# Kernel optimization log

Measured on AMD Instinct MI355X. Metric: run time of the kernel, lower is better.

## Reference

```python
import jax, jax.numpy as jnp
import numpy as np

B, H, S, D = 4, 16, 2048, 64
SCALE = D ** -0.5

def setup_inputs() -> dict:
    key = jax.random.key(0)
    kq, kk, kv = jax.random.split(key, 3)
    q = jax.random.normal(kq, (B, H, S, D), dtype=jnp.float32)
    k = jax.random.normal(kk, (B, H, S, D), dtype=jnp.float32)
    v = jax.random.normal(kv, (B, H, S, D), dtype=jnp.float32)
    return {"q": q, "k": k, "v": v}

def reference(q, k, v):
    # scores: [B, H, S, S]
    scores = jnp.einsum('bhqd,bhkd->bhqk', q, k) * SCALE
    attn = jax.nn.softmax(scores, axis=-1)
    # dropout is identity in eval mode (reference baseline)
    out = jnp.einsum('bhqk,bhkd->bhqd', attn, v)
    return out
```

## Files before the change

### kernel.cpp

```cpp
#include <hip/hip_runtime.h>
#include <hip/hip_bf16.h>


constexpr int Bb = 4, Hh = 16, Ss = 2048, Dd = 64;
constexpr float SCALE_LOG2E = 0.125f * 1.4426950408889634f;
constexpr int KVB = 64;
constexpr int NT = Ss / KVB;

typedef __bf16 bf16x8 __attribute__((ext_vector_type(8)));
typedef float  f32x4  __attribute__((ext_vector_type(4)));
typedef float  f32x16 __attribute__((ext_vector_type(16)));
typedef unsigned int u32x4 __attribute__((ext_vector_type(4)));

__device__ __forceinline__ unsigned cvtpk(float lo, float hi) {
  unsigned r;
  asm("v_cvt_pk_bf16_f32 %0, %1, %2" : "=v"(r) : "v"(lo), "v"(hi));
  return r;
}
__device__ __forceinline__ void permswap(unsigned &a, unsigned &b) {
  asm("v_permlane32_swap_b32 %0, %1" : "+v"(a), "+v"(b));
}

__global__ __launch_bounds__(512, 4)
void sdpa_fwd(const float* __restrict__ Qg, const float* __restrict__ Kg,
              const float* __restrict__ Vg, float* __restrict__ Og) {
  __shared__ __align__(16) char smem[33792];

  const int tid = threadIdx.x;
  const int wave = tid >> 6, lane = tid & 63;
  const int lq = lane & 31, hi = lane >> 5;
  const int swz = (lq & 7) << 4;

  const int bh = blockIdx.x * 8 + (blockIdx.y >> 3);
  const int qt = blockIdx.y & 7;
  const size_t base = (size_t)bh * (Ss * Dd);
  const int qw = qt * 256 + wave * 32;

  const float* Qp = Qg + base;
  const float* Kp = Kg + base;
  const float* Vp = Vg + base;

  const bool isK = (wave < 4);
  const int st  = tid & 255;
  const int skv = st >> 2, s4 = st & 3;
  const int r2  = st >> 3, s8 = st & 7;

  int roff[4];
#pragma unroll
  for (int ds = 0; ds < 4; ++ds) roff[ds] = (32 * ds + 16 * hi) ^ swz;

  bf16x8 qf[4];
  {
    const float* qp = Qp + (size_t)(qw + lq) * Dd;
#pragma unroll
    for (int ds = 0; ds < 4; ++ds) {
      f32x4 x0 = *(const f32x4*)(qp + 16 * ds + 8 * hi);
      f32x4 x1 = *(const f32x4*)(qp + 16 * ds + 8 * hi + 4);
#pragma unroll
      for (int j = 0; j < 4; ++j) {
        qf[ds][j]     = (__bf16)(x0[j] * SCALE_LOG2E);
        qf[ds][j + 4] = (__bf16)(x1[j] * SCALE_LOG2E);
      }
    }
  }

  f32x16 o[2];
#pragma unroll
  for (int a = 0; a < 2; ++a)
#pragma unroll
    for (int i = 0; i < 16; ++i) o[a][i] = 0.f;
  float ps = 0.f;

  f32x4 stg[4];

  auto issue = [&](int t) {
    if (isK) {
      const float* kp = Kp + (size_t)(t * KVB + skv) * Dd + 16 * s4;
#pragma unroll
      for (int i = 0; i < 4; ++i) stg[i] = *(const f32x4*)(kp + 4 * i);
    } else {
      const float* vp = Vp + (size_t)(t * KVB + 2 * r2) * Dd + s8;
#pragma unroll
      for (int j = 0; j < 8; ++j) {
        stg[j >> 2][j & 3]       = vp[8 * j];
        stg[2 + (j >> 2)][j & 3] = vp[Dd + 8 * j];
      }
    }
  };
  auto stage = [&](int buf) {
    char* kb = smem + buf * 8192;
    char* vb = smem + 16384 + buf * 8192;
    if (isK) {
#pragma unroll
      for (int c = 0; c < 2; ++c) {
        bf16x8 w;
#pragma unroll
        for (int j = 0; j < 4; ++j) {
          w[j]     = (__bf16)stg[2 * c][j];
          w[j + 4] = (__bf16)stg[2 * c + 1][j];
        }
        *(bf16x8*)(kb + skv * 128 + 16 * ((2 * s4 + c) ^ (skv & 7))) = w;
      }
    } else {
#pragma unroll
      for (int j = 0; j < 8; ++j) {
        int d = s8 + 8 * j;
        *(unsigned*)(vb + d * 128 + ((4 * r2) ^ ((d & 7) << 4))) =
            cvtpk(stg[j >> 2][j & 3], stg[2 + (j >> 2)][j & 3]);
      }
    }
  };

  issue(0);
  stage(0);
  __syncthreads();

  int pb = 0;
  for (int t = 0; t < NT; ++t) {
    const bool more = (t + 1 < NT);
    if (more) issue(t + 1);

    const char* kb = smem + pb * 8192;
    const char* vb = smem + 16384 + pb * 8192;

#pragma unroll
    for (int kvb = 0; kvb < 2; ++kvb) {
      f32x16 s;
#pragma unroll
      for (int i = 0; i < 16; ++i) s[i] = 0.f;
      __builtin_amdgcn_s_setprio(1);
#pragma unroll
      for (int ds = 0; ds < 4; ++ds) {
        bf16x8 k0 = *(const bf16x8*)(kb + (32 * kvb + lq) * 128 + roff[ds]);
        s = __builtin_amdgcn_mfma_f32_32x32x16_bf16(k0, qf[ds], s, 0, 0, 0);
      }
      __builtin_amdgcn_s_setprio(0);

#pragma unroll
      for (int i = 0; i < 16; ++i) s[i] = __builtin_amdgcn_exp2f(s[i]);
      {
        float u0 = 0.f, u1 = 0.f, u2 = 0.f, u3 = 0.f;
#pragma unroll
        for (int i = 0; i < 16; i += 4) {
          u0 += s[i]; u1 += s[i + 1]; u2 += s[i + 2]; u3 += s[i + 3];
        }
        ps += (u0 + u1) + (u2 + u3);
      }
      bf16x8 pf2[2];
#pragma unroll
      for (int h = 0; h < 2; ++h) {
        const int ofs = 8 * h;
        unsigned x0 = cvtpk(s[ofs + 0], s[ofs + 1]);
        unsigned x1 = cvtpk(s[ofs + 2], s[ofs + 3]);
        unsigned y0 = cvtpk(s[ofs + 4], s[ofs + 5]);
        unsigned y1 = cvtpk(s[ofs + 6], s[ofs + 7]);
        permswap(x0, y0);
        permswap(x1, y1);
        u32x4 w; w[0] = x0; w[1] = x1; w[2] = y0; w[3] = y1;
        pf2[h] = __builtin_bit_cast(bf16x8, w);
      }

      __builtin_amdgcn_s_setprio(1);
#pragma unroll
      for (int c = 0; c < 2; ++c) {
        const int ks = 2 * kvb + c;
        bf16x8 v0 = *(const bf16x8*)(vb + lq * 128        + roff[ks]);
        bf16x8 v1 = *(const bf16x8*)(vb + (32 + lq) * 128 + roff[ks]);
        o[0] = __builtin_amdgcn_mfma_f32_32x32x16_bf16(v0, pf2[c], o[0], 0, 0, 0);
        o[1] = __builtin_amdgcn_mfma_f32_32x32x16_bf16(v1, pf2[c], o[1], 0, 0, 0);
      }
      __builtin_amdgcn_s_setprio(0);
    }

    if (more) stage(1 - pb);
    __syncthreads();
    pb ^= 1;
  }

  const float inv = 1.0f / (ps + __shfl_xor(ps, 32));
  float* ot = (float*)smem + wave * (32 * 33);
  const int q2 = lane >> 1, c2 = lane & 1;
#pragma unroll
  for (int db = 0; db < 2; ++db) {
    const f32x16& acc = o[db];
#pragma unroll
    for (int r = 0; r < 16; ++r)
      ot[lq * 33 + ((r & 3) + 8 * (r >> 2) + 4 * hi)] = acc[r] * inv;
    float* orow = Og + base + (size_t)(qw + q2) * Dd + 32 * db + 16 * c2;
#pragma unroll
    for (int j = 0; j < 4; ++j) {
      f32x4 w;
#pragma unroll
      for (int jj = 0; jj < 4; ++jj) w[jj] = ot[q2 * 33 + 16 * c2 + 4 * j + jj];
      *(f32x4*)(orow + 4 * j) = w;
    }
  }
}

extern "C" void kernel_launch(void* const* d_in, const int* in_sizes, int n_in,
                              void* d_out, int out_size, void* d_ws, size_t ws_size,
                              hipStream_t stream) {
  const float* q = (const float*)d_in[0];
  const float* k = (const float*)d_in[1];
  const float* v = (const float*)d_in[2];
  float* o = (float*)d_out;
  dim3 grid(8, 64);
  sdpa_fwd<<<grid, dim3(512), 0, stream>>>(q, k, v, o);
}
```

Before: 92.35 us.

## Halve block to four waves with each thread loading both K and V tiles

Blocks shrink from 8 waves (256 queries) to 4 waves (128 queries) and the grid doubles to 1024 blocks. Every thread now stages both a K chunk and a V chunk instead of splitting the K and V staging across wave groups. The K conversion uses packed bf16 conversion instructions. This gives more blocks for better CU balance but doubles the K/V global traffic per query, since each KV tile is now shared by fewer queries. It also raises per-thread register pressure, and the occupancy hint changes.

```diff
diff --git a/kernel.cpp b/kernel.cpp
--- a/kernel.cpp
+++ b/kernel.cpp
@@ -21,29 +21,27 @@
   asm("v_permlane32_swap_b32 %0, %1" : "+v"(a), "+v"(b));
 }
 
-__global__ __launch_bounds__(512, 4)
+__global__ __launch_bounds__(256, 3)
 void sdpa_fwd(const float* __restrict__ Qg, const float* __restrict__ Kg,
               const float* __restrict__ Vg, float* __restrict__ Og) {
-  __shared__ __align__(16) char smem[33792];
+  __shared__ __align__(16) char smem[32768];
 
   const int tid = threadIdx.x;
   const int wave = tid >> 6, lane = tid & 63;
   const int lq = lane & 31, hi = lane >> 5;
   const int swz = (lq & 7) << 4;
 
-  const int bh = blockIdx.x * 8 + (blockIdx.y >> 3);
-  const int qt = blockIdx.y & 7;
+  const int bh = blockIdx.x * 8 + (blockIdx.y >> 4);
+  const int qt = blockIdx.y & 15;
   const size_t base = (size_t)bh * (Ss * Dd);
-  const int qw = qt * 256 + wave * 32;
+  const int qw = qt * 128 + wave * 32;
 
   const float* Qp = Qg + base;
   const float* Kp = Kg + base;
   const float* Vp = Vg + base;
 
-  const bool isK = (wave < 4);
-  const int st  = tid & 255;
-  const int skv = st >> 2, s4 = st & 3;
-  const int r2  = st >> 3, s8 = st & 7;
+  const int skv = tid >> 2, s4 = tid & 3;
+  const int r2  = tid >> 3, s8 = tid & 7;
 
   int roff[4];
 #pragma unroll
@@ -71,43 +69,32 @@
     for (int i = 0; i < 16; ++i) o[a][i] = 0.f;
   float ps = 0.f;
 
-  f32x4 stg[4];
+  f32x4 kr[4]; float vA[8], vB[8];
 
   auto issue = [&](int t) {
-    if (isK) {
-      const float* kp = Kp + (size_t)(t * KVB + skv) * Dd + 16 * s4;
+    const float* kp = Kp + (size_t)(t * KVB + skv) * Dd + 16 * s4;
 #pragma unroll
-      for (int i = 0; i < 4; ++i) stg[i] = *(const f32x4*)(kp + 4 * i);
-    } else {
-      const float* vp = Vp + (size_t)(t * KVB + 2 * r2) * Dd + s8;
+    for (int i = 0; i < 4; ++i) kr[i] = *(const f32x4*)(kp + 4 * i);
+    const float* vp = Vp + (size_t)(t * KVB + 2 * r2) * Dd + s8;
 #pragma unroll
-      for (int j = 0; j < 8; ++j) {
-        stg[j >> 2][j & 3]       = vp[8 * j];
-        stg[2 + (j >> 2)][j & 3] = vp[Dd + 8 * j];
-      }
-    }
+    for (int j = 0; j < 8; ++j) { vA[j] = vp[8 * j]; vB[j] = vp[Dd + 8 * j]; }
   };
   auto stage = [&](int buf) {
     char* kb = smem + buf * 8192;
     char* vb = smem + 16384 + buf * 8192;
-    if (isK) {
 #pragma unroll
-      for (int c = 0; c < 2; ++c) {
-        bf16x8 w;
+    for (int c = 0; c < 2; ++c) {
+      u32x4 u;
+      u[0] = cvtpk(kr[2 * c][0], kr[2 * c][1]);
+      u[1] = cvtpk(kr[2 * c][2], kr[2 * c][3]);
+      u[2] = cvtpk(kr[2 * c + 1][0], kr[2 * c + 1][1]);
+      u[3] = cvtpk(kr[2 * c + 1][2], kr[2 * c + 1][3]);
+      *(u32x4*)(kb + skv * 128 + 16 * ((2 * s4 + c) ^ (skv & 7))) = u;
+    }
 #pragma unroll
-        for (int j = 0; j < 4; ++j) {
-          w[j]     = (__bf16)stg[2 * c][j];
-          w[j + 4] = (__bf16)stg[2 * c + 1][j];
-        }
-        *(bf16x8*)(kb + skv * 128 + 16 * ((2 * s4 + c) ^ (skv & 7))) = w;
-      }
-    } else {
-#pragma unroll
-      for (int j = 0; j < 8; ++j) {
-        int d = s8 + 8 * j;
-        *(unsigned*)(vb + d * 128 + ((4 * r2) ^ ((d & 7) << 4))) =
-            cvtpk(stg[j >> 2][j & 3], stg[2 + (j >> 2)][j & 3]);
-      }
+    for (int j = 0; j < 8; ++j) {
+      int d = s8 + 8 * j;
+      *(unsigned*)(vb + d * 128 + ((4 * r2) ^ ((d & 7) << 4))) = cvtpk(vA[j], vB[j]);
     }
   };
 
@@ -204,6 +191,6 @@
   const float* k = (const float*)d_in[1];
   const float* v = (const float*)d_in[2];
   float* o = (float*)d_out;
-  dim3 grid(8, 64);
-  sdpa_fwd<<<grid, dim3(512), 0, stream>>>(q, k, v, o);
+  dim3 grid(8, 128);
+  sdpa_fwd<<<grid, dim3(256), 0, stream>>>(q, k, v, o);
 }
```

Result: slower. 107.9 us (+16.8%).

## Double KV tile to 128 rows with split half-tile prefetch staging

Applied to the files above, without the earlier changes.

Raises the KV tile size from 64 to 128 rows, which halves the number of loop iterations and block-wide barriers. Each tile's global loads are split into two halves whose issue and LDS staging are interleaved between compute quarters, so prefetch latency overlaps with MFMA work without adding staging registers. The V layout in LDS moves to a 256-byte row stride, and K conversion now uses packed cvt instructions. LDS use grows to 64 KB per block, which may reduce the number of resident blocks per CU.

```diff
diff --git a/kernel.cpp b/kernel.cpp
--- a/kernel.cpp
+++ b/kernel.cpp
@@ -4,7 +4,7 @@
 
 constexpr int Bb = 4, Hh = 16, Ss = 2048, Dd = 64;
 constexpr float SCALE_LOG2E = 0.125f * 1.4426950408889634f;
-constexpr int KVB = 64;
+constexpr int KVB = 128;
 constexpr int NT = Ss / KVB;
 
 typedef __bf16 bf16x8 __attribute__((ext_vector_type(8)));
@@ -24,7 +24,7 @@
 __global__ __launch_bounds__(512, 4)
 void sdpa_fwd(const float* __restrict__ Qg, const float* __restrict__ Kg,
               const float* __restrict__ Vg, float* __restrict__ Og) {
-  __shared__ __align__(16) char smem[33792];
+  __shared__ __align__(16) char smem[65536];
 
   const int tid = threadIdx.x;
   const int wave = tid >> 6, lane = tid & 63;
@@ -73,13 +73,14 @@
 
   f32x4 stg[4];
 
-  auto issue = [&](int t) {
+  auto issueH = [&](int t, int half) {
+    const int r0 = t * KVB + 64 * half;
     if (isK) {
-      const float* kp = Kp + (size_t)(t * KVB + skv) * Dd + 16 * s4;
+      const float* kp = Kp + (size_t)(r0 + skv) * Dd + 16 * s4;
 #pragma unroll
       for (int i = 0; i < 4; ++i) stg[i] = *(const f32x4*)(kp + 4 * i);
     } else {
-      const float* vp = Vp + (size_t)(t * KVB + 2 * r2) * Dd + s8;
+      const float* vp = Vp + (size_t)(r0 + 2 * r2) * Dd + s8;
 #pragma unroll
       for (int j = 0; j < 8; ++j) {
         stg[j >> 2][j & 3]       = vp[8 * j];
@@ -87,92 +88,99 @@
       }
     }
   };
-  auto stage = [&](int buf) {
-    char* kb = smem + buf * 8192;
-    char* vb = smem + 16384 + buf * 8192;
+  auto stageH = [&](int buf, int half) {
+    char* kb = smem + buf * 16384;
+    char* vb = smem + 32768 + buf * 16384;
     if (isK) {
+      const int row = 64 * half + skv;
 #pragma unroll
       for (int c = 0; c < 2; ++c) {
-        bf16x8 w;
-#pragma unroll
-        for (int j = 0; j < 4; ++j) {
-          w[j]     = (__bf16)stg[2 * c][j];
-          w[j + 4] = (__bf16)stg[2 * c + 1][j];
-        }
-        *(bf16x8*)(kb + skv * 128 + 16 * ((2 * s4 + c) ^ (skv & 7))) = w;
+        u32x4 u;
+        u[0] = cvtpk(stg[2 * c][0], stg[2 * c][1]);
+        u[1] = cvtpk(stg[2 * c][2], stg[2 * c][3]);
+        u[2] = cvtpk(stg[2 * c + 1][0], stg[2 * c + 1][1]);
+        u[3] = cvtpk(stg[2 * c + 1][2], stg[2 * c + 1][3]);
+        *(u32x4*)(kb + row * 128 + 16 * ((2 * s4 + c) ^ (skv & 7))) = u;
       }
     } else {
+      const int colb = 128 * half + 4 * r2;
 #pragma unroll
       for (int j = 0; j < 8; ++j) {
         int d = s8 + 8 * j;
-        *(unsigned*)(vb + d * 128 + ((4 * r2) ^ ((d & 7) << 4))) =
+        *(unsigned*)(vb + d * 256 + (colb ^ ((d & 7) << 4))) =
             cvtpk(stg[j >> 2][j & 3], stg[2 + (j >> 2)][j & 3]);
       }
     }
   };
 
-  issue(0);
-  stage(0);
+  auto quarter = [&](const char* kb, const char* vb, int kvq) {
+    f32x16 s;
+#pragma unroll
+    for (int i = 0; i < 16; ++i) s[i] = 0.f;
+    __builtin_amdgcn_s_setprio(1);
+#pragma unroll
+    for (int ds = 0; ds < 4; ++ds) {
+      bf16x8 k0 = *(const bf16x8*)(kb + (32 * kvq + lq) * 128 + roff[ds]);
+      s = __builtin_amdgcn_mfma_f32_32x32x16_bf16(k0, qf[ds], s, 0, 0, 0);
+    }
+    __builtin_amdgcn_s_setprio(0);
+
+#pragma unroll
+    for (int i = 0; i < 16; ++i) s[i] = __builtin_amdgcn_exp2f(s[i]);
+    {
+      float u0 = 0.f, u1 = 0.f, u2 = 0.f, u3 = 0.f;
+#pragma unroll
+      for (int i = 0; i < 16; i += 4) {
+        u0 += s[i]; u1 += s[i + 1]; u2 += s[i + 2]; u3 += s[i + 3];
+      }
+      ps += (u0 + u1) + (u2 + u3);
+    }
+    bf16x8 pf2[2];
+#pragma unroll
+    for (int h = 0; h < 2; ++h) {
+      const int ofs = 8 * h;
+      unsigned x0 = cvtpk(s[ofs + 0], s[ofs + 1]);
+      unsigned x1 = cvtpk(s[ofs + 2], s[ofs + 3]);
+      unsigned y0 = cvtpk(s[ofs + 4], s[ofs + 5]);
+      unsigned y1 = cvtpk(s[ofs + 6], s[ofs + 7]);
+      permswap(x0, y0);
+      permswap(x1, y1);
+      u32x4 w; w[0] = x0; w[1] = x1; w[2] = y0; w[3] = y1;
+      pf2[h] = __builtin_bit_cast(bf16x8, w);
+    }
+
+    __builtin_amdgcn_s_setprio(1);
+#pragma unroll
+    for (int c = 0; c < 2; ++c) {
+      const int ks = 2 * kvq + c;
+      const int cb = (32 * ks + 16 * hi) ^ swz;
+      bf16x8 v0 = *(const bf16x8*)(vb + lq * 256        + cb);
+      bf16x8 v1 = *(const bf16x8*)(vb + (32 + lq) * 256 + cb);
+      o[0] = __builtin_amdgcn_mfma_f32_32x32x16_bf16(v0, pf2[c], o[0], 0, 0, 0);
+      o[1] = __builtin_amdgcn_mfma_f32_32x32x16_bf16(v1, pf2[c], o[1], 0, 0, 0);
+    }
+    __builtin_amdgcn_s_setprio(0);
+  };
+
+  issueH(0, 0); stageH(0, 0);
+  issueH(0, 1); stageH(0, 1);
   __syncthreads();
 
   int pb = 0;
   for (int t = 0; t < NT; ++t) {
     const bool more = (t + 1 < NT);
-    if (more) issue(t + 1);
-
-    const char* kb = smem + pb * 8192;
-    const char* vb = smem + 16384 + pb * 8192;
-
-#pragma unroll
-    for (int kvb = 0; kvb < 2; ++kvb) {
-      f32x16 s;
-#pragma unroll
-      for (int i = 0; i < 16; ++i) s[i] = 0.f;
-      __builtin_amdgcn_s_setprio(1);
-#pragma unroll
-      for (int ds = 0; ds < 4; ++ds) {
-        bf16x8 k0 = *(const bf16x8*)(kb + (32 * kvb + lq) * 128 + roff[ds]);
-        s = __builtin_amdgcn_mfma_f32_32x32x16_bf16(k0, qf[ds], s, 0, 0, 0);
-      }
-      __builtin_amdgcn_s_setprio(0);
-
-#pragma unroll
-      for (int i = 0; i < 16; ++i) s[i] = __builtin_amdgcn_exp2f(s[i]);
-      {
-        float u0 = 0.f, u1 = 0.f, u2 = 0.f, u3 = 0.f;
-#pragma unroll
-        for (int i = 0; i < 16; i += 4) {
-          u0 += s[i]; u1 += s[i + 1]; u2 += s[i + 2]; u3 += s[i + 3];
-        }
-        ps += (u0 + u1) + (u2 + u3);
-      }
-      bf16x8 pf2[2];
-#pragma unroll
-      for (int h = 0; h < 2; ++h) {
-        const int ofs = 8 * h;
-        unsigned x0 = cvtpk(s[ofs + 0], s[ofs + 1]);
-        unsigned x1 = cvtpk(s[ofs + 2], s[ofs + 3]);
-        unsigned y0 = cvtpk(s[ofs + 4], s[ofs + 5]);
-        unsigned y1 = cvtpk(s[ofs + 6], s[ofs + 7]);
-        permswap(x0, y0);
-        permswap(x1, y1);
-        u32x4 w; w[0] = x0; w[1] = x1; w[2] = y0; w[3] = y1;
-        pf2[h] = __builtin_bit_cast(bf16x8, w);
-      }
-
-      __builtin_amdgcn_s_setprio(1);
-#pragma unroll
-      for (int c = 0; c < 2; ++c) {
-        const int ks = 2 * kvb + c;
-        bf16x8 v0 = *(const bf16x8*)(vb + lq * 128        + roff[ks]);
-        bf16x8 v1 = *(const bf16x8*)(vb + (32 + lq) * 128 + roff[ks]);
-        o[0] = __builtin_amdgcn_mfma_f32_32x32x16_bf16(v0, pf2[c], o[0], 0, 0, 0);
-        o[1] = __builtin_amdgcn_mfma_f32_32x32x16_bf16(v1, pf2[c], o[1], 0, 0, 0);
-      }
-      __builtin_amdgcn_s_setprio(0);
-    }
-
-    if (more) stage(1 - pb);
+    if (more) issueH(t + 1, 0);
+
+    const char* kb = smem + pb * 16384;
+    const char* vb = smem + 32768 + pb * 16384;
+
+    quarter(kb, vb, 0);
+    quarter(kb, vb, 1);
+    if (more) { stageH(1 - pb, 0); issueH(t + 1, 1); }
+    quarter(kb, vb, 2);
+    quarter(kb, vb, 3);
+    if (more) stageH(1 - pb, 1);
+
     __syncthreads();
     pb ^= 1;
   }
```

After: 214.8 us. +132.6%, slower.
